# Performance work log

Hardware: AMD Instinct MI355X
Metric: run time of the kernel (lower is better)

The kernel has to match this reference:

```python
import jax, jax.numpy as jnp
import numpy as np

N_NODES = 50000
N_EDGES = 600000
EMB = 128

def setup_inputs() -> dict:
    key = jax.random.key(0)
    ks = jax.random.split(key, 6)
    h = jax.random.normal(ks[0], (N_NODES, EMB), dtype=jnp.float32)
    edge_attr = jax.random.normal(ks[1], (N_EDGES, EMB), dtype=jnp.float32)
    src = jax.random.randint(ks[2], (N_EDGES,), 0, N_NODES, dtype=jnp.int32)
    dst = jax.random.randint(ks[3], (N_EDGES,), 0, N_NODES, dtype=jnp.int32)
    # MLP: Linear(emb, 2*emb) -> ReLU -> Linear(2*emb, emb)
    W1 = jax.random.normal(ks[4], (EMB, 2 * EMB), dtype=jnp.float32) * (1.0 / np.sqrt(EMB))
    b1 = jnp.zeros((2 * EMB,), dtype=jnp.float32)
    W2 = jax.random.normal(ks[5], (2 * EMB, EMB), dtype=jnp.float32) * (1.0 / np.sqrt(2 * EMB))
    b2 = jnp.zeros((EMB,), dtype=jnp.float32)
    eps = jnp.zeros((1,), dtype=jnp.float32)
    return {"h": h, "edge_attr": edge_attr, "src": src, "dst": dst,
            "W1": W1, "b1": b1, "W2": W2, "b2": b2, "eps": eps}

def reference(h, edge_attr, src, dst, W1, b1, W2, b2, eps):
    # message: m_e = h[src_e] + edge_attr_e   (edge_encoder is None)
    m = h[src] + edge_attr                              # [E, D]
    # reduce: sum messages per destination node
    aggr = jax.ops.segment_sum(m, dst, num_segments=N_NODES)  # [N, D]
    # out = (1 + eps) * h + MLP(aggr)
    hidden = jax.nn.relu(aggr @ W1 + b1)                # [N, 2D]
    mlp_out = hidden @ W2 + b2                          # [N, D]
    return (1.0 + eps) * h + mlp_out
```

## Files before the change

kernel.cpp:

```cpp
#include <hip/hip_runtime.h>

#define N_NODES 50000
#define N_EDGES 600000
#define D 128
#define H2 256
#define TN 16
#define MAXC 2048

typedef float f4 __attribute__((ext_vector_type(4)));

__device__ __forceinline__ f4 ldg_nt(const float* p) {
    return __builtin_nontemporal_load((const f4*)p);
}
__device__ __forceinline__ f4 ldg(const float* p) {
    return *(const f4*)p;
}

__device__ __forceinline__ unsigned int bfpair(float lo, float hi) {
    unsigned int ul = __float_as_uint(lo), uh = __float_as_uint(hi);
    ul += 0x7FFFu + ((ul >> 16) & 1u);
    uh += 0x7FFFu + ((uh >> 16) & 1u);
    return (ul >> 16) | (uh & 0xFFFF0000u);
}
__device__ __forceinline__ float bflo(unsigned int u) { return __uint_as_float(u << 16); }
__device__ __forceinline__ float bfhi(unsigned int u) { return __uint_as_float(u & 0xFFFF0000u); }

__global__ __launch_bounds__(256) void hist_kernel(const int* __restrict__ dst,
                                                   int* __restrict__ counts) {
    unsigned int e = blockIdx.x * 256u + threadIdx.x;
    if (e < N_EDGES) atomicAdd(&counts[dst[e]], 1);
}

__global__ __launch_bounds__(256) void scan1_kernel(const int* __restrict__ counts,
                                                    int* __restrict__ scanned,
                                                    int* __restrict__ blocksums) {
    __shared__ int wsum[4];
    const int tid = threadIdx.x;
    const int lane = tid & 63;
    const int wv = tid >> 6;
    const int i = blockIdx.x * 256 + tid;
    const int cval = (i < N_NODES) ? counts[i] : 0;
    int x = cval;
    #pragma unroll
    for (int d = 1; d < 64; d <<= 1) {
        int t = __shfl_up(x, d, 64);
        if (lane >= d) x += t;
    }
    if (lane == 63) wsum[wv] = x;
    __syncthreads();
    if (tid == 0) {
        int s = 0;
        #pragma unroll
        for (int w = 0; w < 4; ++w) { s += wsum[w]; wsum[w] = s; }
    }
    __syncthreads();
    const int prefix = (wv > 0 ? wsum[wv - 1] : 0) + (x - cval);
    if (i < N_NODES) scanned[i] = prefix;
    if (tid == 0) blocksums[blockIdx.x] = wsum[3];
}

__global__ __launch_bounds__(256) void scan2_kernel(const int* __restrict__ blocksums,
                                                    int* __restrict__ blockbase, int nb) {
    __shared__ int wsum[4];
    const int tid = threadIdx.x;
    const int lane = tid & 63;
    const int wv = tid >> 6;
    const int cval = (tid < nb) ? blocksums[tid] : 0;
    int x = cval;
    #pragma unroll
    for (int d = 1; d < 64; d <<= 1) {
        int t = __shfl_up(x, d, 64);
        if (lane >= d) x += t;
    }
    if (lane == 63) wsum[wv] = x;
    __syncthreads();
    if (tid == 0) {
        int s = 0;
        #pragma unroll
        for (int w = 0; w < 4; ++w) { s += wsum[w]; wsum[w] = s; }
    }
    __syncthreads();
    if (tid < nb) blockbase[tid] = (wv > 0 ? wsum[wv - 1] : 0) + (x - cval);
}

__global__ __launch_bounds__(256) void scan3_kernel(const int* __restrict__ scanned,
                                                    const int* __restrict__ blockbase,
                                                    int* __restrict__ offsets,
                                                    int* __restrict__ cursor) {
    const int i = blockIdx.x * 256 + threadIdx.x;
    if (i < N_NODES) {
        const int v = scanned[i] + blockbase[blockIdx.x];
        offsets[i] = v;
        cursor[i] = v;
    }
    if (i == 0) offsets[N_NODES] = N_EDGES;
}

__global__ __launch_bounds__(256) void scatter_kernel(const int* __restrict__ src,
                                                      const int* __restrict__ dst,
                                                      int* __restrict__ cursor,
                                                      int2* __restrict__ perm2) {
    unsigned int e = blockIdx.x * 256u + threadIdx.x;
    if (e >= N_EDGES) return;
    const int d = dst[e];
    const int p = atomicAdd(&cursor[d], 1);
    perm2[p] = make_int2((int)e, src[e]);
}

__global__ __launch_bounds__(256, 8) void fused_kernel(
    const float* __restrict__ h, const float* __restrict__ ea,
    const int* __restrict__ offsets, const int2* __restrict__ perm2,
    const float* __restrict__ W1, const float* __restrict__ b1,
    const float* __restrict__ W2, const float* __restrict__ b2,
    const float* __restrict__ eps, float* __restrict__ out)
{
    __shared__ float s_lds[5120];
    int2* s_perm = (int2*)s_lds;
    unsigned int* s_aggr = (unsigned int*)s_lds;
    float* s_w = s_lds + 1024;
    unsigned int* s_hid = (unsigned int*)(s_lds + 3072);

    const int tid = threadIdx.x;
    const int t  = tid >> 4;
    const int c8 = (tid & 15) << 3;
    const int node0 = blockIdx.x * TN;
    const int blkbeg = offsets[node0];
    const int blkend = offsets[node0 + TN];
    const int nbeg = offsets[node0 + t];
    const int nend = offsets[node0 + t + 1];

    f4 a0 = (f4)(0.f);
    f4 a1 = (f4)(0.f);

    for (int cb = blkbeg; cb < blkend; cb += MAXC) {
        const int cnt = min(blkend - cb, MAXC);
        __syncthreads();
        for (int i = tid; i < cnt; i += 256) s_perm[i] = perm2[cb + i];
        __syncthreads();
        const int lo = max(nbeg - cb, 0);
        const int hi = min(nend - cb, cnt);
        int j = lo;
        for (; j + 3 < hi; j += 4) {
            int2 p[4];
            #pragma unroll
            for (int q = 0; q < 4; ++q) p[q] = s_perm[j + q];
            f4 ev0[4], ev1[4], hv0[4], hv1[4];
            #pragma unroll
            for (int q = 0; q < 4; ++q) {
                const float* er = ea + (size_t)p[q].x * D + c8;
                const float* hr = h  + (size_t)p[q].y * D + c8;
                ev0[q] = ldg_nt(er);
                ev1[q] = ldg_nt(er + 4);
                hv0[q] = ldg(hr);
                hv1[q] = ldg(hr + 4);
            }
            #pragma unroll
            for (int q = 0; q < 4; ++q) {
                a0 += ev0[q] + hv0[q];
                a1 += ev1[q] + hv1[q];
            }
        }
        for (; j < hi; ++j) {
            const int2 p = s_perm[j];
            const float* er = ea + (size_t)p.x * D + c8;
            const float* hr = h  + (size_t)p.y * D + c8;
            a0 += ldg_nt(er)     + ldg(hr);
            a1 += ldg_nt(er + 4) + ldg(hr + 4);
        }
    }
    __syncthreads();
    {
        unsigned int* ad = s_aggr + t * 64 + (c8 >> 1);
        ad[0] = bfpair(a0[0], a0[1]);
        ad[1] = bfpair(a0[2], a0[3]);
        ad[2] = bfpair(a1[0], a1[1]);
        ad[3] = bfpair(a1[2], a1[3]);
    }

    const int j0 = (tid & 63) << 2;
    const int tbase = (tid >> 6) << 2;
    {
        float4 acc1[4];
        const float4 bv = *(const float4*)(b1 + j0);
        #pragma unroll
        for (int q = 0; q < 4; ++q) acc1[q] = bv;
        for (int k0 = 0; k0 < D; k0 += 8) {
            __syncthreads();
            {
                const float4* srcw = (const float4*)(W1 + (size_t)k0 * H2);
                float4* dstl = (float4*)s_w;
                dstl[tid]       = srcw[tid];
                dstl[tid + 256] = srcw[tid + 256];
            }
            __syncthreads();
            #pragma unroll
            for (int kk = 0; kk < 8; kk += 4) {
                float4 w[4];
                #pragma unroll
                for (int q = 0; q < 4; ++q)
                    w[q] = *(const float4*)&s_w[(kk + q) * H2 + j0];
                #pragma unroll
                for (int u = 0; u < 4; ++u) {
                    const unsigned int* ar = s_aggr + (tbase + u) * 64 + ((k0 + kk) >> 1);
                    const unsigned int u01 = ar[0];
                    const unsigned int u23 = ar[1];
                    float4 a;
                    a.x = bflo(u01); a.y = bfhi(u01);
                    a.z = bflo(u23); a.w = bfhi(u23);
                    acc1[u].x = fmaf(a.x, w[0].x, acc1[u].x);
                    acc1[u].y = fmaf(a.x, w[0].y, acc1[u].y);
                    acc1[u].z = fmaf(a.x, w[0].z, acc1[u].z);
                    acc1[u].w = fmaf(a.x, w[0].w, acc1[u].w);
                    acc1[u].x = fmaf(a.y, w[1].x, acc1[u].x);
                    acc1[u].y = fmaf(a.y, w[1].y, acc1[u].y);
                    acc1[u].z = fmaf(a.y, w[1].z, acc1[u].z);
                    acc1[u].w = fmaf(a.y, w[1].w, acc1[u].w);
                    acc1[u].x = fmaf(a.z, w[2].x, acc1[u].x);
                    acc1[u].y = fmaf(a.z, w[2].y, acc1[u].y);
                    acc1[u].z = fmaf(a.z, w[2].z, acc1[u].z);
                    acc1[u].w = fmaf(a.z, w[2].w, acc1[u].w);
                    acc1[u].x = fmaf(a.w, w[3].x, acc1[u].x);
                    acc1[u].y = fmaf(a.w, w[3].y, acc1[u].y);
                    acc1[u].z = fmaf(a.w, w[3].z, acc1[u].z);
                    acc1[u].w = fmaf(a.w, w[3].w, acc1[u].w);
                }
            }
        }
        #pragma unroll
        for (int u = 0; u < 4; ++u) {
            unsigned int* hd = s_hid + (tbase + u) * 128 + (j0 >> 1);
            hd[0] = bfpair(fmaxf(acc1[u].x, 0.f), fmaxf(acc1[u].y, 0.f));
            hd[1] = bfpair(fmaxf(acc1[u].z, 0.f), fmaxf(acc1[u].w, 0.f));
        }
    }

    {
        const int i0 = (tid & 31) << 2;
        const int g = tid >> 5;
        float4 acc2[2];
        const float4 bv = *(const float4*)(b2 + i0);
        acc2[0] = bv; acc2[1] = bv;
        for (int k0 = 0; k0 < H2; k0 += 16) {
            __syncthreads();
            {
                const float4* srcw = (const float4*)(W2 + (size_t)k0 * D);
                float4* dstl = (float4*)s_w;
                dstl[tid]       = srcw[tid];
                dstl[tid + 256] = srcw[tid + 256];
            }
            __syncthreads();
            #pragma unroll
            for (int kk = 0; kk < 16; kk += 4) {
                float4 w[4];
                #pragma unroll
                for (int q = 0; q < 4; ++q)
                    w[q] = *(const float4*)&s_w[(kk + q) * D + i0];
                #pragma unroll
                for (int u = 0; u < 2; ++u) {
                    const unsigned int* hr = s_hid + (g + u * 8) * 128 + ((k0 + kk) >> 1);
                    const unsigned int u01 = hr[0];
                    const unsigned int u23 = hr[1];
                    float4 a;
                    a.x = bflo(u01); a.y = bfhi(u01);
                    a.z = bflo(u23); a.w = bfhi(u23);
                    acc2[u].x = fmaf(a.x, w[0].x, acc2[u].x);
                    acc2[u].y = fmaf(a.x, w[0].y, acc2[u].y);
                    acc2[u].z = fmaf(a.x, w[0].z, acc2[u].z);
                    acc2[u].w = fmaf(a.x, w[0].w, acc2[u].w);
                    acc2[u].x = fmaf(a.y, w[1].x, acc2[u].x);
                    acc2[u].y = fmaf(a.y, w[1].y, acc2[u].y);
                    acc2[u].z = fmaf(a.y, w[1].z, acc2[u].z);
                    acc2[u].w = fmaf(a.y, w[1].w, acc2[u].w);
                    acc2[u].x = fmaf(a.z, w[2].x, acc2[u].x);
                    acc2[u].y = fmaf(a.z, w[2].y, acc2[u].y);
                    acc2[u].z = fmaf(a.z, w[2].z, acc2[u].z);
                    acc2[u].w = fmaf(a.z, w[2].w, acc2[u].w);
                    acc2[u].x = fmaf(a.w, w[3].x, acc2[u].x);
                    acc2[u].y = fmaf(a.w, w[3].y, acc2[u].y);
                    acc2[u].z = fmaf(a.w, w[3].z, acc2[u].z);
                    acc2[u].w = fmaf(a.w, w[3].w, acc2[u].w);
                }
            }
        }
        const float ep = 1.0f + eps[0];
        #pragma unroll
        for (int u = 0; u < 2; ++u) {
            const int node = node0 + g + u * 8;
            const f4 hv = ldg(h + (size_t)node * D + i0);
            f4 o;
            o[0] = fmaf(ep, hv[0], acc2[u].x);
            o[1] = fmaf(ep, hv[1], acc2[u].y);
            o[2] = fmaf(ep, hv[2], acc2[u].z);
            o[3] = fmaf(ep, hv[3], acc2[u].w);
            __builtin_nontemporal_store(o, (f4*)(out + (size_t)node * D + i0));
        }
    }
}

extern "C" void kernel_launch(void* const* d_in, const int* in_sizes, int n_in,
                              void* d_out, int out_size, void* d_ws, size_t ws_size,
                              hipStream_t stream) {
    const float* h   = (const float*)d_in[0];
    const float* ea  = (const float*)d_in[1];
    const int*   src = (const int*)d_in[2];
    const int*   dst = (const int*)d_in[3];
    const float* W1  = (const float*)d_in[4];
    const float* b1  = (const float*)d_in[5];
    const float* W2  = (const float*)d_in[6];
    const float* b2  = (const float*)d_in[7];
    const float* eps = (const float*)d_in[8];
    float* out = (float*)d_out;

    char* ws = (char*)d_ws;
    int*  counts    = (int*)ws;
    int*  scanned   = (int*)(ws + 256 * 1024);
    int*  offsets   = (int*)(ws + 512 * 1024);
    int*  cursor    = (int*)(ws + 768 * 1024);
    int*  blocksums = (int*)(ws + 1008 * 1024);
    int*  blockbase = (int*)(ws + 1012 * 1024);
    int2* perm2     = (int2*)(ws + 1024 * 1024);

    hipMemsetAsync(counts, 0, N_NODES * sizeof(int), stream);

    const int eblocks = (N_EDGES + 255) / 256;
    const int nblocks = (N_NODES + 255) / 256;

    hist_kernel<<<eblocks, 256, 0, stream>>>(dst, counts);
    scan1_kernel<<<nblocks, 256, 0, stream>>>(counts, scanned, blocksums);
    scan2_kernel<<<1, 256, 0, stream>>>(blocksums, blockbase, nblocks);
    scan3_kernel<<<nblocks, 256, 0, stream>>>(scanned, blockbase, offsets, cursor);
    scatter_kernel<<<eblocks, 256, 0, stream>>>(src, dst, cursor, perm2);
    fused_kernel<<<N_NODES / TN, 256, 0, stream>>>(
        h, ea, offsets, perm2, W1, b1, W2, b2, eps, out);
}
```

Baseline: 594.6 us.

## Gather source node features from a bf16 copy of h in the edge aggregation

```diff
diff --git a/kernel.cpp b/kernel.cpp
--- a/kernel.cpp
+++ b/kernel.cpp
@@ -8,6 +8,7 @@
 #define MAXC 2048
 
 typedef float f4 __attribute__((ext_vector_type(4)));
+typedef unsigned int u4 __attribute__((ext_vector_type(4)));
 
 __device__ __forceinline__ f4 ldg_nt(const float* p) {
     return __builtin_nontemporal_load((const f4*)p);
@@ -24,6 +25,21 @@
 }
 __device__ __forceinline__ float bflo(unsigned int u) { return __uint_as_float(u << 16); }
 __device__ __forceinline__ float bfhi(unsigned int u) { return __uint_as_float(u & 0xFFFF0000u); }
+
+__global__ __launch_bounds__(256) void hcvt_kernel(const float* __restrict__ h,
+                                                   u4* __restrict__ hb4) {
+    const int i = blockIdx.x * 256 + threadIdx.x;
+    if (i < (N_NODES * D) / 8) {
+        const f4 v0 = ldg(h + (size_t)i * 8);
+        const f4 v1 = ldg(h + (size_t)i * 8 + 4);
+        u4 o;
+        o.x = bfpair(v0[0], v0[1]);
+        o.y = bfpair(v0[2], v0[3]);
+        o.z = bfpair(v1[0], v1[1]);
+        o.w = bfpair(v1[2], v1[3]);
+        hb4[i] = o;
+    }
+}
 
 __global__ __launch_bounds__(256) void hist_kernel(const int* __restrict__ dst,
                                                    int* __restrict__ counts) {
@@ -104,11 +120,12 @@
     if (e >= N_EDGES) return;
     const int d = dst[e];
     const int p = atomicAdd(&cursor[d], 1);
-    perm2[p] = make_int2((int)e, src[e]);
-}
-
-__global__ __launch_bounds__(256, 8) void fused_kernel(
+    perm2[p] = make_int2((int)(e * D), src[e] * D);
+}
+
+__global__ __launch_bounds__(256, 6) void fused_kernel(
     const float* __restrict__ h, const float* __restrict__ ea,
+    const unsigned int* __restrict__ hb,
     const int* __restrict__ offsets, const int2* __restrict__ perm2,
     const float* __restrict__ W1, const float* __restrict__ b1,
     const float* __restrict__ W2, const float* __restrict__ b2,
@@ -144,28 +161,39 @@
             int2 p[4];
             #pragma unroll
             for (int q = 0; q < 4; ++q) p[q] = s_perm[j + q];
-            f4 ev0[4], ev1[4], hv0[4], hv1[4];
+            f4 ev0[4], ev1[4];
+            u4 hu[4];
             #pragma unroll
             for (int q = 0; q < 4; ++q) {
-                const float* er = ea + (size_t)p[q].x * D + c8;
-                const float* hr = h  + (size_t)p[q].y * D + c8;
+                const float* er = ea + (size_t)(unsigned)p[q].x + c8;
                 ev0[q] = ldg_nt(er);
                 ev1[q] = ldg_nt(er + 4);
-                hv0[q] = ldg(hr);
-                hv1[q] = ldg(hr + 4);
+                hu[q]  = *(const u4*)(hb + (((unsigned)p[q].y + c8) >> 1));
             }
             #pragma unroll
             for (int q = 0; q < 4; ++q) {
-                a0 += ev0[q] + hv0[q];
-                a1 += ev1[q] + hv1[q];
+                f4 hv0, hv1;
+                hv0[0] = bflo(hu[q].x); hv0[1] = bfhi(hu[q].x);
+                hv0[2] = bflo(hu[q].y); hv0[3] = bfhi(hu[q].y);
+                hv1[0] = bflo(hu[q].z); hv1[1] = bfhi(hu[q].z);
+                hv1[2] = bflo(hu[q].w); hv1[3] = bfhi(hu[q].w);
+                a0 += ev0[q] + hv0;
+                a1 += ev1[q] + hv1;
             }
         }
         for (; j < hi; ++j) {
             const int2 p = s_perm[j];
-            const float* er = ea + (size_t)p.x * D + c8;
-            const float* hr = h  + (size_t)p.y * D + c8;
-            a0 += ldg_nt(er)     + ldg(hr);
-            a1 += ldg_nt(er + 4) + ldg(hr + 4);
+            const float* er = ea + (size_t)(unsigned)p.x + c8;
+            const f4 e0 = ldg_nt(er);
+            const f4 e1 = ldg_nt(er + 4);
+            const u4 u = *(const u4*)(hb + (((unsigned)p.y + c8) >> 1));
+            f4 hv0, hv1;
+            hv0[0] = bflo(u.x); hv0[1] = bfhi(u.x);
+            hv0[2] = bflo(u.y); hv0[3] = bfhi(u.y);
+            hv1[0] = bflo(u.z); hv1[1] = bfhi(u.z);
+            hv1[2] = bflo(u.w); hv1[3] = bfhi(u.w);
+            a0 += e0 + hv0;
+            a1 += e1 + hv1;
         }
     }
     __syncthreads();
@@ -319,17 +347,19 @@
     int*  blocksums = (int*)(ws + 1008 * 1024);
     int*  blockbase = (int*)(ws + 1012 * 1024);
     int2* perm2     = (int2*)(ws + 1024 * 1024);
+    unsigned int* hbm = (unsigned int*)(ws + 6 * 1024 * 1024);
 
     hipMemsetAsync(counts, 0, N_NODES * sizeof(int), stream);
 
     const int eblocks = (N_EDGES + 255) / 256;
     const int nblocks = (N_NODES + 255) / 256;
 
+    hcvt_kernel<<<(N_NODES * D / 8 + 255) / 256, 256, 0, stream>>>(h, (u4*)hbm);
     hist_kernel<<<eblocks, 256, 0, stream>>>(dst, counts);
     scan1_kernel<<<nblocks, 256, 0, stream>>>(counts, scanned, blocksums);
     scan2_kernel<<<1, 256, 0, stream>>>(blocksums, blockbase, nblocks);
     scan3_kernel<<<nblocks, 256, 0, stream>>>(scanned, blockbase, offsets, cursor);
     scatter_kernel<<<eblocks, 256, 0, stream>>>(src, dst, cursor, perm2);
     fused_kernel<<<N_NODES / TN, 256, 0, stream>>>(
-        h, ea, offsets, perm2, W1, b1, W2, b2, eps, out);
-}
+        h, ea, hbm, offsets, perm2, W1, b1, W2, b2, eps, out);
+}
```

After: 583.1 us. No clear change (-1.9%).
